# Kernel tuning notes

Measured on AMD Instinct MI355X. Metric: run time of the kernel, lower is better.

Reference implementation:

```python
import jax, jax.numpy as jnp
import numpy as np

IN_FEATURES = 512
OUT_FEATURES = 512
B_EXP = 2.0
EPS = 1e-12  # torch F.normalize eps


def setup_inputs() -> dict:
    key = jax.random.key(0)
    kz, kw = jax.random.split(key)
    z = jax.random.normal(kz, (100000, IN_FEATURES), dtype=jnp.float32)
    weight = jax.random.normal(kw, (OUT_FEATURES, IN_FEATURES), dtype=jnp.float32) * (1.0 / np.sqrt(IN_FEATURES))
    return {"z": z, "weight": weight}


def reference(z, weight):
    # lin = z @ W^T : [N, out]
    lin = jnp.einsum('ni,oi->no', z, weight)
    # row-wise L2 normalize (torch F.normalize: x / max(||x||, eps))
    z_norm = z / jnp.maximum(jnp.linalg.norm(z, axis=1, keepdims=True), EPS)
    w_norm = weight / jnp.maximum(jnp.linalg.norm(weight, axis=1, keepdims=True), EPS)
    cos = jnp.einsum('ni,oi->no', z_norm, w_norm)
    scale = jnp.abs(cos) ** (B_EXP - 1.0)
    return lin * scale
```

## Files before the change

kernel.cpp:

```cpp
#include <hip/hip_runtime.h>
#include <hip/hip_bf16.h>
#include <stdint.h>


constexpr int KDIM = 512;
constexpr int NDIM = 512;

typedef __attribute__((ext_vector_type(8))) short bf16x8;
typedef __attribute__((ext_vector_type(4))) float f32x4;

__device__ __forceinline__ uint32_t pk_bf16(float a, float b) {
  __hip_bfloat162 h = __float22bfloat162_rn(make_float2(a, b));
  union { __hip_bfloat162 h2; uint32_t u; } c;
  c.h2 = h;
  return c.u;
}

__global__ __launch_bounds__(128) void prep_w(const float* __restrict__ w,
                                              unsigned short* __restrict__ wb,
                                              float* __restrict__ cninv) {
  const int row = blockIdx.x;
  const int t   = threadIdx.x;
  const float* gp = w + (size_t)row * KDIM + t * 4;
  f32x4 v = *(const f32x4*)gp;
  float s = v.x * v.x + v.y * v.y + v.z * v.z + v.w * v.w;

  uint2 p;
  p.x = pk_bf16(v.x, v.y);
  p.y = pk_bf16(v.z, v.w);
  *(uint2*)(wb + (size_t)row * KDIM + t * 4) = p;

  #pragma unroll
  for (int off = 32; off > 0; off >>= 1) s += __shfl_down(s, off, 64);
  __shared__ float red[2];
  if ((t & 63) == 0) red[t >> 6] = s;
  __syncthreads();
  if (t == 0) cninv[row] = 1.0f / fmaxf(sqrtf(red[0] + red[1]), 1e-12f);
}

__global__ __launch_bounds__(512, 4) void gemm_bcos(const float* __restrict__ z,
                                                    const unsigned short* __restrict__ wb,
                                                    const float* __restrict__ cninv,
                                                    float* __restrict__ out, int M) {
  __shared__ unsigned short As[64 * 512];
  __shared__ float rowsq[64];
  __shared__ float rinv[64];

  const int t    = threadIdx.x;
  const int w    = t >> 6;
  const int lane = t & 63;
  const int lrow = lane & 15;
  const int quad = lane >> 4;
  const int mb   = blockIdx.x;
  const int wn   = w * 64;

  #pragma unroll
  for (int rr = 0; rr < 8; ++rr) {
    const int rl = w * 8 + rr;
    int rg = mb * 64 + rl;
    if (rg >= M) rg = M - 1;
    const float* zp = z + (size_t)rg * KDIM;
    float s = 0.0f;
    #pragma unroll
    for (int j = 0; j < 2; ++j) {
      f32x4 v = __builtin_nontemporal_load((const f32x4*)(zp + j * 256 + lane * 4));
      s += v.x * v.x + v.y * v.y + v.z * v.z + v.w * v.w;
      uint2 p;
      p.x = pk_bf16(v.x, v.y);
      p.y = pk_bf16(v.z, v.w);
      const int cb = (j * 512 + lane * 8) ^ (rr << 4);
      *(uint2*)((char*)As + rl * 1024 + cb) = p;
    }
    #pragma unroll
    for (int off = 32; off > 0; off >>= 1) s += __shfl_down(s, off, 64);
    if (lane == 0) rowsq[rl] = s;
  }
  __syncthreads();
  if (t < 64) rinv[t] = 1.0f / fmaxf(sqrtf(rowsq[t]), 1e-12f);
  __syncthreads();

  f32x4 acc[4][4];
  #pragma unroll
  for (int i = 0; i < 4; ++i)
    #pragma unroll
    for (int j = 0; j < 4; ++j) acc[i][j] = (f32x4)0.0f;

  const int qs = (quad * 16) ^ ((lrow & 7) << 4);
  const unsigned short* wbp = wb + (size_t)(wn + lrow) * KDIM + quad * 8;

  #pragma unroll 2
  for (int ks = 0; ks < 16; ++ks) {
    bf16x8 a[4], b[4];
    #pragma unroll
    for (int nt = 0; nt < 4; ++nt)
      b[nt] = *(const bf16x8*)(wbp + nt * 16 * KDIM + ks * 32);
    #pragma unroll
    for (int mt = 0; mt < 4; ++mt)
      a[mt] = *(const bf16x8*)((const char*)As + ((mt * 16 + lrow) << 10) + ((ks * 64) ^ qs));
    #pragma unroll
    for (int mt = 0; mt < 4; ++mt)
      #pragma unroll
      for (int nt = 0; nt < 4; ++nt)
        acc[mt][nt] = __builtin_amdgcn_mfma_f32_16x16x32_bf16(a[mt], b[nt], acc[mt][nt], 0, 0, 0);
  }

  #pragma unroll
  for (int nt = 0; nt < 4; ++nt) {
    const int colg = wn + nt * 16 + lrow;
    const float cv = cninv[colg];
    #pragma unroll
    for (int mt = 0; mt < 4; ++mt) {
      const int rl = mt * 16 + quad * 4;
      #pragma unroll
      for (int i = 0; i < 4; ++i) {
        const int rowg = mb * 64 + rl + i;
        if (rowg < M) {
          const float v = acc[mt][nt][i];
          __builtin_nontemporal_store(v * fabsf(v) * rinv[rl + i] * cv,
                                      &out[(size_t)rowg * NDIM + colg]);
        }
      }
    }
  }
}

extern "C" void kernel_launch(void* const* d_in, const int* in_sizes, int n_in,
                              void* d_out, int out_size, void* d_ws, size_t ws_size,
                              hipStream_t stream) {
  const float* z = (const float*)d_in[0];
  const float* w = (const float*)d_in[1];
  float* out = (float*)d_out;
  const int M = in_sizes[0] / KDIM;

  unsigned short* wb = (unsigned short*)d_ws;
  float* cninv = (float*)((char*)d_ws + (size_t)NDIM * KDIM * 2);

  prep_w<<<dim3(NDIM), dim3(128), 0, stream>>>(w, wb, cninv);

  dim3 grid((M + 63) / 64);
  gemm_bcos<<<grid, dim3(512), 0, stream>>>(z, wb, cninv, out, M);
}
```

Measured before the change: 444.8 us.

## Stage weight chunks in LDS via double-buffered async global-to-LDS loads

Rewrites the weight layout so each 32-wide K chunk is stored contiguously, then streams those chunks into a double-buffered LDS region with global_load_lds while the MFMA loop consumes the previous chunk. A-fragment reads from LDS are also software-prefetched one step ahead, and MFMA sections run at raised wave priority. This replaces per-wave direct global reads of B with shared staging. In exchange it adds 64KB more LDS per block, which lowers occupancy (launch bounds drop to 2 blocks), and puts two barriers in every K step.

```diff
diff --git a/kernel.cpp b/kernel.cpp
--- a/kernel.cpp
+++ b/kernel.cpp
@@ -16,19 +16,28 @@
   return c.u;
 }
 
+__device__ __forceinline__ void gload_lds16(const void* g, void* lds) {
+  __builtin_amdgcn_global_load_lds(
+      (const __attribute__((address_space(1))) uint32_t*)(uintptr_t)g,
+      (__attribute__((address_space(3))) uint32_t*)(uintptr_t)lds,
+      16, 0, 0);
+}
+
 __global__ __launch_bounds__(128) void prep_w(const float* __restrict__ w,
-                                              unsigned short* __restrict__ wb,
+                                              unsigned short* __restrict__ wbt,
                                               float* __restrict__ cninv) {
   const int row = blockIdx.x;
   const int t   = threadIdx.x;
-  const float* gp = w + (size_t)row * KDIM + t * 4;
-  f32x4 v = *(const f32x4*)gp;
+  const int k0  = t * 4;
+  f32x4 v = *(const f32x4*)(w + (size_t)row * KDIM + k0);
   float s = v.x * v.x + v.y * v.y + v.z * v.z + v.w * v.w;
 
   uint2 p;
   p.x = pk_bf16(v.x, v.y);
   p.y = pk_bf16(v.z, v.w);
-  *(uint2*)(wb + (size_t)row * KDIM + t * 4) = p;
+  const int c  = k0 >> 5;
+  const int k8 = (k0 >> 3) & 3;
+  *(uint2*)(wbt + ((size_t)c * 2048 + k8 * 512 + row) * 8 + (k0 & 7)) = p;
 
   #pragma unroll
   for (int off = 32; off > 0; off >>= 1) s += __shfl_down(s, off, 64);
@@ -38,13 +47,14 @@
   if (t == 0) cninv[row] = 1.0f / fmaxf(sqrtf(red[0] + red[1]), 1e-12f);
 }
 
-__global__ __launch_bounds__(512, 4) void gemm_bcos(const float* __restrict__ z,
-                                                    const unsigned short* __restrict__ wb,
+__global__ __launch_bounds__(512, 2) void gemm_bcos(const float* __restrict__ z,
+                                                    const unsigned short* __restrict__ wbt,
                                                     const float* __restrict__ cninv,
                                                     float* __restrict__ out, int M) {
   __shared__ unsigned short As[64 * 512];
+  __shared__ unsigned short Bs[2][2048 * 8];
   __shared__ float rowsq[64];
-  __shared__ float rinv[64];
+  __shared__ float rinv_s[64];
 
   const int t    = threadIdx.x;
   const int w    = t >> 6;
@@ -55,6 +65,13 @@
   const int wn   = w * 64;
 
   #pragma unroll
+  for (int i = 0; i < 4; ++i)
+    gload_lds16(wbt + (size_t)(t + 512 * i) * 8, &Bs[0][(t + 512 * i) * 8]);
+  #pragma unroll
+  for (int i = 0; i < 4; ++i)
+    gload_lds16(wbt + (size_t)(2048 + t + 512 * i) * 8, &Bs[1][(t + 512 * i) * 8]);
+
+  #pragma unroll
   for (int rr = 0; rr < 8; ++rr) {
     const int rl = w * 8 + rr;
     int rg = mb * 64 + rl;
@@ -63,7 +80,7 @@
     float s = 0.0f;
     #pragma unroll
     for (int j = 0; j < 2; ++j) {
-      f32x4 v = __builtin_nontemporal_load((const f32x4*)(zp + j * 256 + lane * 4));
+      f32x4 v = *(const f32x4*)(zp + j * 256 + lane * 4);
       s += v.x * v.x + v.y * v.y + v.z * v.z + v.w * v.w;
       uint2 p;
       p.x = pk_bf16(v.x, v.y);
@@ -76,7 +93,7 @@
     if (lane == 0) rowsq[rl] = s;
   }
   __syncthreads();
-  if (t < 64) rinv[t] = 1.0f / fmaxf(sqrtf(rowsq[t]), 1e-12f);
+  if (t < 64) rinv_s[t] = 1.0f / fmaxf(sqrtf(rowsq[t]), 1e-12f);
   __syncthreads();
 
   f32x4 acc[4][4];
@@ -86,22 +103,46 @@
     for (int j = 0; j < 4; ++j) acc[i][j] = (f32x4)0.0f;
 
   const int qs = (quad * 16) ^ ((lrow & 7) << 4);
-  const unsigned short* wbp = wb + (size_t)(wn + lrow) * KDIM + quad * 8;
 
-  #pragma unroll 2
-  for (int ks = 0; ks < 16; ++ks) {
-    bf16x8 a[4], b[4];
+  bf16x8 a[2][4];
+  #pragma unroll
+  for (int mt = 0; mt < 4; ++mt)
+    a[0][mt] = *(const bf16x8*)((const char*)As + ((mt * 16 + lrow) << 10) + (0 ^ qs));
+
+  #pragma unroll
+  for (int c = 0; c < 16; ++c) {
+    if (c < 15) asm volatile("s_waitcnt vmcnt(4)" ::: "memory");
+    else        asm volatile("s_waitcnt vmcnt(0)" ::: "memory");
+    __builtin_amdgcn_s_barrier();
+    asm volatile("" ::: "memory");
+
+    bf16x8 b[4];
     #pragma unroll
     for (int nt = 0; nt < 4; ++nt)
-      b[nt] = *(const bf16x8*)(wbp + nt * 16 * KDIM + ks * 32);
-    #pragma unroll
-    for (int mt = 0; mt < 4; ++mt)
-      a[mt] = *(const bf16x8*)((const char*)As + ((mt * 16 + lrow) << 10) + ((ks * 64) ^ qs));
+      b[nt] = *(const bf16x8*)&Bs[c & 1][(quad * 512 + wn + nt * 16 + lrow) * 8];
+    if (c < 15) {
+      #pragma unroll
+      for (int mt = 0; mt < 4; ++mt)
+        a[(c + 1) & 1][mt] = *(const bf16x8*)((const char*)As +
+            ((mt * 16 + lrow) << 10) + (((c + 1) * 64) ^ qs));
+    }
+
+    __builtin_amdgcn_s_setprio(1);
     #pragma unroll
     for (int mt = 0; mt < 4; ++mt)
       #pragma unroll
       for (int nt = 0; nt < 4; ++nt)
-        acc[mt][nt] = __builtin_amdgcn_mfma_f32_16x16x32_bf16(a[mt], b[nt], acc[mt][nt], 0, 0, 0);
+        acc[mt][nt] = __builtin_amdgcn_mfma_f32_16x16x32_bf16(a[c & 1][mt], b[nt], acc[mt][nt], 0, 0, 0);
+    __builtin_amdgcn_s_setprio(0);
+
+    asm volatile("" ::: "memory");
+    __builtin_amdgcn_s_barrier();
+    if (c + 2 < 16) {
+      #pragma unroll
+      for (int i = 0; i < 4; ++i)
+        gload_lds16(wbt + ((size_t)(c + 2) * 2048 + t + 512 * i) * 8,
+                    &Bs[c & 1][(t + 512 * i) * 8]);
+    }
   }
 
   #pragma unroll
@@ -116,7 +157,7 @@
         const int rowg = mb * 64 + rl + i;
         if (rowg < M) {
           const float v = acc[mt][nt][i];
-          __builtin_nontemporal_store(v * fabsf(v) * rinv[rl + i] * cv,
+          __builtin_nontemporal_store(v * fabsf(v) * rinv_s[rl + i] * cv,
                                       &out[(size_t)rowg * NDIM + colg]);
         }
       }
@@ -132,11 +173,11 @@
   float* out = (float*)d_out;
   const int M = in_sizes[0] / KDIM;
 
-  unsigned short* wb = (unsigned short*)d_ws;
+  unsigned short* wbt = (unsigned short*)d_ws;
   float* cninv = (float*)((char*)d_ws + (size_t)NDIM * KDIM * 2);
 
-  prep_w<<<dim3(NDIM), dim3(128), 0, stream>>>(w, wb, cninv);
+  prep_w<<<dim3(NDIM), dim3(128), 0, stream>>>(w, wbt, cninv);
 
   dim3 grid((M + 63) / 64);
-  gemm_bcos<<<grid, dim3(512), 0, stream>>>(z, wb, cninv, out, M);
+  gemm_bcos<<<grid, dim3(512), 0, stream>>>(z, wbt, cninv, out, M);
 }
```

New measurement: 422.7 us. 1.05x faster.
